# Kernel tuning notes

Measured on AMD Instinct MI355X. Metric: run time of the kernel, lower is better.

The kernel has to match this reference:

```python
import jax, jax.numpy as jnp
import numpy as np

NCONF, NATOMS, NSTATES = 8, 10, 4
NBASIS, HIDDEN, NTYPES = 24, 48, 4
CUTOFF = 6.0
FACTOR_KIN = 0.5
ALPHA = 1.5
PI = 3.141592653589793


def _make_pairs():
    # all ordered (i, j) pairs of distinct atoms within each configuration,
    # indices into the flattened [nconf*natoms] atom axis
    idx = []
    for c in range(NCONF):
        base = c * NATOMS
        for i in range(NATOMS):
            for j in range(NATOMS):
                if i != j:
                    idx.append((base + i, base + j))
    return np.asarray(idx, dtype=np.int32).T  # [2, npairs]


def setup_inputs():
    key = jax.random.key(0)
    ks = jax.random.split(key, 9)
    cart = 0.8 * jax.random.normal(ks[0], (NCONF, NATOMS, 3), jnp.float32)
    species = jax.random.randint(ks[1], (NCONF, NATOMS), 0, NTYPES, dtype=jnp.int32)
    massrev = jax.random.uniform(ks[2], (NCONF, NATOMS), jnp.float32, 0.5, 1.5)
    pot = jax.random.normal(ks[3], (NCONF,), jnp.float32)
    eigen_weight = jax.random.normal(ks[4], (NSTATES,), jnp.float32)
    atom_index = jnp.asarray(_make_pairs())
    shifts = jnp.zeros((atom_index.shape[1], 3), jnp.float32)
    numatoms = jnp.full((NCONF,), NATOMS, dtype=jnp.int32)
    W1 = jax.random.normal(ks[5], (NBASIS, HIDDEN), jnp.float32) / np.sqrt(NBASIS).astype(np.float32)
    B1 = 0.1 * jax.random.normal(ks[6], (NTYPES, HIDDEN), jnp.float32)
    W2 = jax.random.normal(ks[7], (HIDDEN, NSTATES), jnp.float32) / np.sqrt(HIDDEN).astype(np.float32)
    Emb = 0.1 * jax.random.normal(ks[8], (NTYPES, NSTATES), jnp.float32)
    elevel = jnp.linspace(0.5, 2.0, NSTATES).astype(jnp.float32)
    return dict(eigen_weight=eigen_weight, pot=pot, cart=cart, numatoms=numatoms,
                species=species, massrev=massrev, atom_index=atom_index,
                shifts=shifts, W1=W1, B1=B1, W2=W2, Emb=Emb, elevel=elevel)


def _get_wave(cart, species_flat, atom_index, shifts, W1, B1, W2, Emb):
    # psi_density: gaussian RBF x cosine cutoff, scattered to center atoms
    nconf, natoms, _ = cart.shape
    na = nconf * natoms
    flat = cart.reshape(na, 3)
    dvec = flat[atom_index[1]] + shifts - flat[atom_index[0]]   # [npairs, 3]
    dist = jnp.sqrt(jnp.sum(dvec * dvec, axis=-1))              # [npairs]
    centers = jnp.linspace(0.0, CUTOFF, NBASIS).astype(cart.dtype)
    fcut = 0.5 * (jnp.cos(PI * jnp.minimum(dist, CUTOFF) / CUTOFF) + 1.0)
    rbf = jnp.exp(-ALPHA * jnp.square(dist[:, None] - centers[None, :])) * fcut[:, None]
    density = jax.ops.segment_sum(rbf, atom_index[0], num_segments=na)   # [na, NBASIS]
    # psi_nnmod: species-conditioned MLP
    h = jnp.tanh(density @ W1 + B1[species_flat])
    initpsi = h @ W2 + Emb[species_flat]                        # [na, NSTATES]
    # wavefunction assembly: gather neighbor psi, weight by radial, scatter-add
    radial = jnp.sin(dist * (PI / CUTOFF)) ** 3                 # [npairs]
    expand_psi = initpsi[atom_index[1]] * radial[:, None]       # [npairs, NSTATES]
    atompsi = jax.ops.segment_sum(expand_psi, atom_index[0], num_segments=na)
    tmppsi = atompsi.reshape(nconf, natoms, -1).sum(axis=1)     # [nconf, NSTATES]
    psi = jnp.concatenate([jnp.square(tmppsi[:, :1]), tmppsi[:, 1:]], axis=1)
    return psi


def reference(eigen_weight, pot, cart, numatoms, species, massrev, atom_index,
              shifts, W1, B1, W2, Emb, elevel):
    species_flat = species.reshape(-1)
    wave = lambda c: _get_wave(c, species_flat, atom_index, shifts, W1, B1, W2, Emb)
    psi = wave(cart)                                  # [nconf, NSTATES]
    potene = pot - pot[-1]                            # get_abpot

    sumwave = lambda c: wave(c).sum(axis=0)           # [NSTATES]

    def get_jac(c):
        jac = jax.jacrev(sumwave)(c)                  # [S, nconf, natoms, 3]
        return jac.sum(axis=1)                        # [S, natoms, 3]

    operator_psi = jax.jacfwd(get_jac)(cart)          # [S, natoms, 3, nconf, natoms, 3]
    part_sum = jnp.einsum('jmliml->jmi', operator_psi)            # diagonal trace terms
    kin_psi = -jnp.einsum('jmi,im->ij', part_sum, massrev) * FACTOR_KIN  # [nconf, S]
    pot_psi = psi * potene[:, None]
    vibene = (kin_psi + pot_psi) / psi
    return jnp.sum(jnp.square(vibene - elevel[None, :]))
```

## Files before the change

### kernel.cpp

```cpp
#include <hip/hip_runtime.h>

#define NCONF   8
#define NATOMS  10
#define NSTATES 4
#define NBASIS  24
#define HIDDEN  48
#define NPAIRC  90
#define NNEI    9
#define NDIR    30
#define CUTOFF  6.0f
#define ALPHA   1.5f
#define PI_F    3.14159265358979323846f


__device__ __forceinline__ float fast_tanh(float x) {
    return 1.0f - 2.0f / (__expf(2.0f * x) + 1.0f);
}

__global__ __launch_bounds__(256) void jet_kernel(
    const float* __restrict__ cart,
    const int*   __restrict__ species,
    const float* __restrict__ massrev,
    const int*   __restrict__ ai,
    const float* __restrict__ shifts,
    const float* __restrict__ W1,
    const float* __restrict__ B1,
    const float* __restrict__ W2,
    const float* __restrict__ Emb,
    int npairs,
    float* __restrict__ ws)
{
    __shared__ float cartc[NATOMS][3];
    __shared__ int   spec[NATOMS];
    __shared__ int   cnt[NATOMS], dcnt[NATOMS];
    __shared__ int   plist[NATOMS][NNEI];
    __shared__ int   dlist[NATOMS][NNEI];
    __shared__ float pJ[NPAIRC][9];
    __shared__ float RJ[NATOMS][3];
    __shared__ float denJ[NATOMS][NBASIS][3];
    __shared__ float hJ[NATOMS][HIDDEN][3];
    __shared__ float psJ[NATOMS][NSTATES][3];
    __shared__ float W1s[NBASIS * HIDDEN];

    const int tid = threadIdx.x;
    const int c   = blockIdx.x / NDIR;
    const int d   = blockIdx.x % NDIR;
    const int m   = d / 3, l = d % 3;

    if (tid < NATOMS*3) cartc[tid/3][tid%3] = cart[c*NATOMS*3 + tid];
    if (tid < NATOMS)   { spec[tid] = species[c*NATOMS + tid]; cnt[tid] = 0; dcnt[tid] = 0; }
    for (int t = tid; t < NBASIS*HIDDEN; t += 256) W1s[t] = W1[t];
    __syncthreads();

    const float kc = PI_F / CUTOFF;

    if (tid < NPAIRC) {
        const int p  = tid;
        const int pg = c*NPAIRC + p;
        const int i = ai[pg]          - c*NATOMS;
        const int j = ai[npairs + pg] - c*NATOMS;
        plist[i][atomicAdd(&cnt[i], 1)]  = p;
        dlist[j][atomicAdd(&dcnt[j], 1)] = p;
        const float sg = (float)((j == m) - (i == m));
        const float dv0 = cartc[j][0] + shifts[pg*3+0] - cartc[i][0];
        const float dv1 = cartc[j][1] + shifts[pg*3+1] - cartc[i][1];
        const float dv2 = cartc[j][2] + shifts[pg*3+2] - cartc[i][2];
        const float dvl = (l == 0) ? dv0 : (l == 1) ? dv1 : dv2;
        const float r2v = dv0*dv0 + dv1*dv1 + dv2*dv2;
        const float r2g = 2.f*dvl*sg;
        const float r2h = 2.f*sg*sg;
        const float dvv = __fsqrt_rn(r2v);
        const float inv = 0.5f / dvv;
        const float dg  = r2g * inv;
        const float dh  = r2h * inv - 0.25f * r2g * r2g / (r2v * dvv);
        const float u  = kc * dvv;
        const float su = __sinf(u), cu = __cosf(u);
        const float r1  = 3.f*su*su*cu*kc;
        const float r2d = kc*kc*(6.f*su*cu*cu - 3.f*su*su*su);
        float dcv, dcg, dch;
        if (dvv < CUTOFF) { dcv = dvv; dcg = dg; dch = dh; }
        else              { dcv = CUTOFF; dcg = 0.f; dch = 0.f; }
        const float uc = kc * dcv;
        const float fv = 0.5f*(__cosf(uc) + 1.f);
        const float f1 = -0.5f*kc*__sinf(uc);
        const float f2 = -0.5f*kc*kc*__cosf(uc);
        pJ[p][0] = dvv; pJ[p][1] = dg;            pJ[p][2] = dh;
        pJ[p][3] = fv;  pJ[p][4] = f1*dcg;        pJ[p][5] = f1*dch + f2*dcg*dcg;
        pJ[p][6] = su*su*su;
        pJ[p][7] = r1*dg;
        pJ[p][8] = r1*dh + r2d*dg*dg;
    }
    __syncthreads();

    if (tid < NATOMS*NBASIS) {
        const int a = tid / NBASIS, b = tid % NBASIS;
        const float cb = (CUTOFF/23.0f) * (float)b;
        float s0 = 0.f, s1 = 0.f, s2 = 0.f;
        #pragma unroll
        for (int k = 0; k < NNEI; ++k) {
            const int p = plist[a][k];
            const float dvv = pJ[p][0], dg = pJ[p][1], dh = pJ[p][2];
            const float fv  = pJ[p][3], fg = pJ[p][4], fh = pJ[p][5];
            const float t  = dvv - cb;
            const float ev = __expf(-ALPHA*t*t);
            const float e1 = -2.f*ALPHA*t*ev;
            const float e2 = (-2.f*ALPHA + 4.f*ALPHA*ALPHA*t*t)*ev;
            const float eg = e1*dg;
            const float eh = e1*dh + e2*dg*dg;
            s0 += ev*fv;
            s1 += ev*fg + eg*fv;
            s2 += ev*fh + 2.f*eg*fg + eh*fv;
        }
        denJ[a][b][0] = s0; denJ[a][b][1] = s1; denJ[a][b][2] = s2;
    } else if (tid < NATOMS*NBASIS + NATOMS) {
        const int j = tid - NATOMS*NBASIS;
        float r0 = 0.f, r1 = 0.f, r2 = 0.f;
        #pragma unroll
        for (int k = 0; k < NNEI; ++k) {
            const int p = dlist[j][k];
            r0 += pJ[p][6]; r1 += pJ[p][7]; r2 += pJ[p][8];
        }
        RJ[j][0] = r0; RJ[j][1] = r1; RJ[j][2] = r2;
    }
    __syncthreads();

    for (int task = tid; task < NATOMS*HIDDEN; task += 256) {
        const int a = task / HIDDEN, hd = task % HIDDEN;
        float v = B1[spec[a]*HIDDEN + hd], g = 0.f, hh = 0.f;
        #pragma unroll
        for (int b = 0; b < NBASIS; ++b) {
            const float w = W1s[b*HIDDEN + hd];
            v  += denJ[a][b][0]*w;
            g  += denJ[a][b][1]*w;
            hh += denJ[a][b][2]*w;
        }
        const float y  = fast_tanh(v);
        const float y1 = 1.f - y*y;
        hJ[a][hd][0] = y;
        hJ[a][hd][1] = y1*g;
        hJ[a][hd][2] = y1*hh - 2.f*y*y1*g*g;
    }
    __syncthreads();

    if (tid < NATOMS*NSTATES) {
        const int a = tid / NSTATES, s = tid % NSTATES;
        float v = Emb[spec[a]*NSTATES + s], g = 0.f, hh = 0.f;
        #pragma unroll
        for (int hd = 0; hd < HIDDEN; ++hd) {
            const float w = W2[hd*NSTATES + s];
            v  += hJ[a][hd][0]*w;
            g  += hJ[a][hd][1]*w;
            hh += hJ[a][hd][2]*w;
        }
        psJ[a][s][0] = v; psJ[a][s][1] = g; psJ[a][s][2] = hh;
    }
    __syncthreads();

    if (tid < NSTATES) {
        const int s = tid;
        float t = 0.f, g = 0.f, hh = 0.f;
        #pragma unroll
        for (int j = 0; j < NATOMS; ++j) {
            const float rv = RJ[j][0], rg = RJ[j][1], rh = RJ[j][2];
            const float iv = psJ[j][s][0], ig = psJ[j][s][1], ih = psJ[j][s][2];
            t  += iv*rv;
            g  += iv*rg + ig*rv;
            hh += iv*rh + 2.f*ig*rg + ih*rv;
        }
        float pv, ph;
        if (s == 0) { pv = t*t; ph = 2.f*(t*hh + g*g); }
        else        { pv = t;   ph = hh; }
        ws[(c*NDIR + d)*NSTATES + s] = massrev[c*NATOMS + m] * ph;
        if (d == 0) ws[NCONF*NDIR*NSTATES + c*NSTATES + s] = pv;
    }
}

__global__ __launch_bounds__(64) void finish_kernel(
    const float* __restrict__ ws,
    const float* __restrict__ pot,
    const float* __restrict__ elevel,
    float* __restrict__ out)
{
    const int t = threadIdx.x;
    float val = 0.f;
    if (t < NCONF*NSTATES) {
        const int c = t / NSTATES, s = t % NSTATES;
        float kin = 0.f;
        #pragma unroll
        for (int d = 0; d < NDIR; ++d) kin += ws[(c*NDIR + d)*NSTATES + s];
        kin *= -0.5f;
        const float psi    = ws[NCONF*NDIR*NSTATES + c*NSTATES + s];
        const float potene = pot[c] - pot[NCONF-1];
        const float vib    = (kin + psi*potene) / psi;
        const float e      = vib - elevel[s];
        val = e*e;
    }
    #pragma unroll
    for (int off = 32; off > 0; off >>= 1) val += __shfl_down(val, off, 64);
    if (t == 0) out[0] = val;
}

extern "C" void kernel_launch(void* const* d_in, const int* in_sizes, int n_in,
                              void* d_out, int out_size, void* d_ws, size_t ws_size,
                              hipStream_t stream) {
    const float* pot     = (const float*)d_in[1];
    const float* cart    = (const float*)d_in[2];
    const int*   species = (const int*)  d_in[4];
    const float* massrev = (const float*)d_in[5];
    const int*   ai      = (const int*)  d_in[6];
    const float* shifts  = (const float*)d_in[7];
    const float* W1      = (const float*)d_in[8];
    const float* B1      = (const float*)d_in[9];
    const float* W2      = (const float*)d_in[10];
    const float* Emb     = (const float*)d_in[11];
    const float* elevel  = (const float*)d_in[12];
    const int npairs = in_sizes[6] / 2;

    float* ws = (float*)d_ws;

    jet_kernel<<<NCONF*NDIR, 256, 0, stream>>>(cart, species, massrev, ai, shifts,
                                               W1, B1, W2, Emb, npairs, ws);
    finish_kernel<<<1, 64, 0, stream>>>(ws, pot, elevel, (float*)d_out);
}
```

Measured before the change: 84.05 us.

## Assign one wavefront per atom and replace block barriers with wave fences

Each block now runs 640 threads, one 64-lane wavefront per atom. Each wave handles its own atom's pairs, density, hidden layer and output layer, separated by wave-level barriers instead of block-wide __syncthreads. The pair list is no longer read from atom_index. It is derived from the fixed all-pairs ordering, so the atomics and neighbour-list construction are gone. W1 is now read straight from global memory instead of being staged in LDS. This depends on the input pair layout always being the complete ordered pair set, and it leaves many lanes idle in each wave.

```diff
diff --git a/kernel.cpp b/kernel.cpp
--- a/kernel.cpp
+++ b/kernel.cpp
@@ -13,58 +13,51 @@
 #define PI_F    3.14159265358979323846f
 
 
+__device__ __forceinline__ void wave_fence() {
+    __builtin_amdgcn_wave_barrier();
+    asm volatile("" ::: "memory");
+}
+
 __device__ __forceinline__ float fast_tanh(float x) {
     return 1.0f - 2.0f / (__expf(2.0f * x) + 1.0f);
 }
 
-__global__ __launch_bounds__(256) void jet_kernel(
+__global__ __launch_bounds__(640) void jet_kernel(
     const float* __restrict__ cart,
     const int*   __restrict__ species,
     const float* __restrict__ massrev,
-    const int*   __restrict__ ai,
     const float* __restrict__ shifts,
     const float* __restrict__ W1,
     const float* __restrict__ B1,
     const float* __restrict__ W2,
     const float* __restrict__ Emb,
-    int npairs,
     float* __restrict__ ws)
 {
-    __shared__ float cartc[NATOMS][3];
-    __shared__ int   spec[NATOMS];
-    __shared__ int   cnt[NATOMS], dcnt[NATOMS];
-    __shared__ int   plist[NATOMS][NNEI];
-    __shared__ int   dlist[NATOMS][NNEI];
-    __shared__ float pJ[NPAIRC][9];
-    __shared__ float RJ[NATOMS][3];
+    __shared__ float pJ[NATOMS][NNEI][9];
     __shared__ float denJ[NATOMS][NBASIS][3];
     __shared__ float hJ[NATOMS][HIDDEN][3];
     __shared__ float psJ[NATOMS][NSTATES][3];
-    __shared__ float W1s[NBASIS * HIDDEN];
-
-    const int tid = threadIdx.x;
-    const int c   = blockIdx.x / NDIR;
-    const int d   = blockIdx.x % NDIR;
-    const int m   = d / 3, l = d % 3;
-
-    if (tid < NATOMS*3) cartc[tid/3][tid%3] = cart[c*NATOMS*3 + tid];
-    if (tid < NATOMS)   { spec[tid] = species[c*NATOMS + tid]; cnt[tid] = 0; dcnt[tid] = 0; }
-    for (int t = tid; t < NBASIS*HIDDEN; t += 256) W1s[t] = W1[t];
-    __syncthreads();
-
+    __shared__ float RJ[NATOMS][3];
+
+    const int tid  = threadIdx.x;
+    const int a    = tid >> 6;
+    const int lane = tid & 63;
+    const int c    = blockIdx.x / NDIR;
+    const int d    = blockIdx.x % NDIR;
+    const int m    = d / 3, l = d % 3;
     const float kc = PI_F / CUTOFF;
 
-    if (tid < NPAIRC) {
-        const int p  = tid;
-        const int pg = c*NPAIRC + p;
-        const int i = ai[pg]          - c*NATOMS;
-        const int j = ai[npairs + pg] - c*NATOMS;
-        plist[i][atomicAdd(&cnt[i], 1)]  = p;
-        dlist[j][atomicAdd(&dcnt[j], 1)] = p;
-        const float sg = (float)((j == m) - (i == m));
-        const float dv0 = cartc[j][0] + shifts[pg*3+0] - cartc[i][0];
-        const float dv1 = cartc[j][1] + shifts[pg*3+1] - cartc[i][1];
-        const float dv2 = cartc[j][2] + shifts[pg*3+2] - cartc[i][2];
+    const int   spc  = species[c*NATOMS + a];
+    const float mrev = massrev[c*NATOMS + m];
+
+    if (lane < NNEI) {
+        const int k  = lane;
+        const int j  = (k < a) ? k : k + 1;
+        const int pg = c*NPAIRC + a*NNEI + k;
+        const float sg = (float)((j == m) - (a == m));
+        const float dv0 = cart[c*NATOMS*3 + j*3 + 0] + shifts[pg*3+0] - cart[c*NATOMS*3 + a*3 + 0];
+        const float dv1 = cart[c*NATOMS*3 + j*3 + 1] + shifts[pg*3+1] - cart[c*NATOMS*3 + a*3 + 1];
+        const float dv2 = cart[c*NATOMS*3 + j*3 + 2] + shifts[pg*3+2] - cart[c*NATOMS*3 + a*3 + 2];
         const float dvl = (l == 0) ? dv0 : (l == 1) ? dv1 : dv2;
         const float r2v = dv0*dv0 + dv1*dv1 + dv2*dv2;
         const float r2g = 2.f*dvl*sg;
@@ -84,23 +77,22 @@
         const float fv = 0.5f*(__cosf(uc) + 1.f);
         const float f1 = -0.5f*kc*__sinf(uc);
         const float f2 = -0.5f*kc*kc*__cosf(uc);
-        pJ[p][0] = dvv; pJ[p][1] = dg;            pJ[p][2] = dh;
-        pJ[p][3] = fv;  pJ[p][4] = f1*dcg;        pJ[p][5] = f1*dch + f2*dcg*dcg;
-        pJ[p][6] = su*su*su;
-        pJ[p][7] = r1*dg;
-        pJ[p][8] = r1*dh + r2d*dg*dg;
-    }
-    __syncthreads();
-
-    if (tid < NATOMS*NBASIS) {
-        const int a = tid / NBASIS, b = tid % NBASIS;
+        pJ[a][k][0] = dvv; pJ[a][k][1] = dg;      pJ[a][k][2] = dh;
+        pJ[a][k][3] = fv;  pJ[a][k][4] = f1*dcg;  pJ[a][k][5] = f1*dch + f2*dcg*dcg;
+        pJ[a][k][6] = su*su*su;
+        pJ[a][k][7] = r1*dg;
+        pJ[a][k][8] = r1*dh + r2d*dg*dg;
+    }
+    wave_fence();
+
+    if (lane < NBASIS) {
+        const int b = lane;
         const float cb = (CUTOFF/23.0f) * (float)b;
         float s0 = 0.f, s1 = 0.f, s2 = 0.f;
         #pragma unroll
         for (int k = 0; k < NNEI; ++k) {
-            const int p = plist[a][k];
-            const float dvv = pJ[p][0], dg = pJ[p][1], dh = pJ[p][2];
-            const float fv  = pJ[p][3], fg = pJ[p][4], fh = pJ[p][5];
+            const float dvv = pJ[a][k][0], dg = pJ[a][k][1], dh = pJ[a][k][2];
+            const float fv  = pJ[a][k][3], fg = pJ[a][k][4], fh = pJ[a][k][5];
             const float t  = dvv - cb;
             const float ev = __expf(-ALPHA*t*t);
             const float e1 = -2.f*ALPHA*t*ev;
@@ -112,24 +104,15 @@
             s2 += ev*fh + 2.f*eg*fg + eh*fv;
         }
         denJ[a][b][0] = s0; denJ[a][b][1] = s1; denJ[a][b][2] = s2;
-    } else if (tid < NATOMS*NBASIS + NATOMS) {
-        const int j = tid - NATOMS*NBASIS;
-        float r0 = 0.f, r1 = 0.f, r2 = 0.f;
-        #pragma unroll
-        for (int k = 0; k < NNEI; ++k) {
-            const int p = dlist[j][k];
-            r0 += pJ[p][6]; r1 += pJ[p][7]; r2 += pJ[p][8];
-        }
-        RJ[j][0] = r0; RJ[j][1] = r1; RJ[j][2] = r2;
-    }
-    __syncthreads();
-
-    for (int task = tid; task < NATOMS*HIDDEN; task += 256) {
-        const int a = task / HIDDEN, hd = task % HIDDEN;
-        float v = B1[spec[a]*HIDDEN + hd], g = 0.f, hh = 0.f;
+    }
+    wave_fence();
+
+    if (lane < HIDDEN) {
+        const int hd = lane;
+        float v = B1[spc*HIDDEN + hd], g = 0.f, hh = 0.f;
         #pragma unroll
         for (int b = 0; b < NBASIS; ++b) {
-            const float w = W1s[b*HIDDEN + hd];
+            const float w = W1[b*HIDDEN + hd];
             v  += denJ[a][b][0]*w;
             g  += denJ[a][b][1]*w;
             hh += denJ[a][b][2]*w;
@@ -140,11 +123,11 @@
         hJ[a][hd][1] = y1*g;
         hJ[a][hd][2] = y1*hh - 2.f*y*y1*g*g;
     }
-    __syncthreads();
-
-    if (tid < NATOMS*NSTATES) {
-        const int a = tid / NSTATES, s = tid % NSTATES;
-        float v = Emb[spec[a]*NSTATES + s], g = 0.f, hh = 0.f;
+    wave_fence();
+
+    if (lane < NSTATES) {
+        const int s = lane;
+        float v = Emb[spc*NSTATES + s], g = 0.f, hh = 0.f;
         #pragma unroll
         for (int hd = 0; hd < HIDDEN; ++hd) {
             const float w = W2[hd*NSTATES + s];
@@ -154,8 +137,21 @@
         }
         psJ[a][s][0] = v; psJ[a][s][1] = g; psJ[a][s][2] = hh;
     }
+
     __syncthreads();
 
+    if (tid < NATOMS) {
+        const int j = tid;
+        float r0 = 0.f, r1 = 0.f, r2 = 0.f;
+        #pragma unroll
+        for (int i = 0; i < NATOMS; ++i) {
+            if (i == j) continue;
+            const int k = (j < i) ? j : j - 1;
+            r0 += pJ[i][k][6]; r1 += pJ[i][k][7]; r2 += pJ[i][k][8];
+        }
+        RJ[j][0] = r0; RJ[j][1] = r1; RJ[j][2] = r2;
+    }
+    wave_fence();
     if (tid < NSTATES) {
         const int s = tid;
         float t = 0.f, g = 0.f, hh = 0.f;
@@ -170,7 +166,7 @@
         float pv, ph;
         if (s == 0) { pv = t*t; ph = 2.f*(t*hh + g*g); }
         else        { pv = t;   ph = hh; }
-        ws[(c*NDIR + d)*NSTATES + s] = massrev[c*NATOMS + m] * ph;
+        ws[(c*NDIR + d)*NSTATES + s] = mrev * ph;
         if (d == 0) ws[NCONF*NDIR*NSTATES + c*NSTATES + s] = pv;
     }
 }
@@ -207,18 +203,16 @@
     const float* cart    = (const float*)d_in[2];
     const int*   species = (const int*)  d_in[4];
     const float* massrev = (const float*)d_in[5];
-    const int*   ai      = (const int*)  d_in[6];
     const float* shifts  = (const float*)d_in[7];
     const float* W1      = (const float*)d_in[8];
     const float* B1      = (const float*)d_in[9];
     const float* W2      = (const float*)d_in[10];
     const float* Emb     = (const float*)d_in[11];
     const float* elevel  = (const float*)d_in[12];
-    const int npairs = in_sizes[6] / 2;
 
     float* ws = (float*)d_ws;
 
-    jet_kernel<<<NCONF*NDIR, 256, 0, stream>>>(cart, species, massrev, ai, shifts,
-                                               W1, B1, W2, Emb, npairs, ws);
+    jet_kernel<<<NCONF*NDIR, 640, 0, stream>>>(cart, species, massrev, shifts,
+                                               W1, B1, W2, Emb, ws);
     finish_kernel<<<1, 64, 0, stream>>>(ws, pot, elevel, (float*)d_out);
 }
```

Result: no change. 84.66 us (+0.7%).
